# Optimization experiments

Measured on AMD Instinct MI355X. Metric: run time of the kernel, lower is better.

The kernel has to match this reference:

```python
import jax, jax.numpy as jnp
import numpy as np
from jax import lax

C_RED = 32
IN_CH = 256
BN_EPS = 1e-5
NORM_EPS = 1e-6


def setup_inputs() -> dict:
    key = jax.random.key(0)
    ks = jax.random.split(key, 5)
    B, H, W = 16, 64, 64
    x = jax.random.normal(ks[0], (B, IN_CH, H, W), dtype=jnp.float32)
    w_reduce = jax.random.normal(ks[1], (C_RED, IN_CH), dtype=jnp.float32) * 0.05
    bn_gamma = jnp.ones((C_RED,), dtype=jnp.float32)
    bn_beta = jnp.zeros((C_RED,), dtype=jnp.float32)
    bn_mean = jax.random.normal(ks[2], (C_RED,), dtype=jnp.float32) * 0.1
    bn_var = jax.random.uniform(ks[3], (C_RED,), dtype=jnp.float32, minval=0.5, maxval=1.5)
    # depthwise 3x3 kernel, OIHW with I=1 (groups == channels)
    dw_weight = jax.random.normal(ks[4], (C_RED, 1, 3, 3), dtype=jnp.float32) * 0.1
    scale = jnp.ones((C_RED,), dtype=jnp.float32)
    return {"x": x, "w_reduce": w_reduce, "bn_gamma": bn_gamma, "bn_beta": bn_beta,
            "bn_mean": bn_mean, "bn_var": bn_var, "dw_weight": dw_weight, "scale": scale}


def _l2_normalize(t):
    # F.normalize(p=2, dim=1, eps=1e-6): divide by max(||t||_2, eps) along channel dim
    n = jnp.sqrt(jnp.sum(t * t, axis=1, keepdims=True))
    return t / jnp.maximum(n, NORM_EPS)


def reference(x, w_reduce, bn_gamma, bn_beta, bn_mean, bn_var, dw_weight, scale):
    # 1x1 reduce conv (no bias)
    z = jnp.einsum('bihw,oi->bohw', x, w_reduce)
    # BatchNorm2d (inference: running stats)
    inv = bn_gamma / jnp.sqrt(bn_var + BN_EPS)
    z = z * inv[None, :, None, None] + (bn_beta - bn_mean * inv)[None, :, None, None]
    z = jax.nn.relu(z)
    # SpiralTwist: depthwise 3x3 conv (SAME) then per-channel scale
    z_tw = lax.conv_general_dilated(
        z, dw_weight, window_strides=(1, 1), padding='SAME',
        feature_group_count=C_RED,
        dimension_numbers=('NCHW', 'OIHW', 'NCHW'))
    z_tw = z_tw * scale[None, :, None, None]
    z_norm = _l2_normalize(z)
    z_tw_norm = _l2_normalize(z_tw)
    # upper-triangular channel pairs (i <= j)
    idx_i, idx_j = np.triu_indices(C_RED, k=0)
    pair = z_norm[:, idx_i] * z_tw_norm[:, idx_j]  # [B, C*(C+1)/2, H, W]
    return jnp.concatenate([z_norm, pair], axis=1)
```

## Files before the change

### kernel.cpp

```cpp
#include <hip/hip_runtime.h>
#include <stdint.h>

#define CIN  256
#define CR   32
#define COUT 560

__global__ __launch_bounds__(512) void k_conv1x1(
    const float* __restrict__ x,
    const float* __restrict__ wr,
    const float* __restrict__ gamma,
    const float* __restrict__ beta,
    const float* __restrict__ mean,
    const float* __restrict__ var,
    float* __restrict__ z)
{
    const int tid = threadIdx.x;
    const int og  = __builtin_amdgcn_readfirstlane(tid >> 6);
    const int q   = tid & 63;
    const int blk = blockIdx.x;
    const int b   = blk >> 4;
    const int p0  = (blk & 15) << 8;

    const float* xb = x + ((((size_t)b) * CIN) << 12) + p0 + (q << 2);
    const float* wp = wr + og * 4 * CIN;

    float4 a0 = {0.f,0.f,0.f,0.f};
    float4 a1 = {0.f,0.f,0.f,0.f};
    float4 a2 = {0.f,0.f,0.f,0.f};
    float4 a3 = {0.f,0.f,0.f,0.f};

    float4 xv0[16], xv1[16];

#define LOADCH(buf, cc)                                                      \
    _Pragma("unroll")                                                        \
    for (int k = 0; k < 16; ++k)                                             \
        buf[k] = *(const float4*)(xb + ((size_t)((cc) * 16 + k) << 12));

#define FMACH(buf, cc)                                                       \
    _Pragma("unroll")                                                        \
    for (int k = 0; k < 16; ++k) {                                           \
        const int ic = (cc) * 16 + k;                                        \
        const float w0 = wp[           ic];                                  \
        const float w1 = wp[    CIN  + ic];                                  \
        const float w2 = wp[2 * CIN  + ic];                                  \
        const float w3 = wp[3 * CIN  + ic];                                  \
        a0.x = fmaf(buf[k].x, w0, a0.x);  a0.y = fmaf(buf[k].y, w0, a0.y);   \
        a0.z = fmaf(buf[k].z, w0, a0.z);  a0.w = fmaf(buf[k].w, w0, a0.w);   \
        a1.x = fmaf(buf[k].x, w1, a1.x);  a1.y = fmaf(buf[k].y, w1, a1.y);   \
        a1.z = fmaf(buf[k].z, w1, a1.z);  a1.w = fmaf(buf[k].w, w1, a1.w);   \
        a2.x = fmaf(buf[k].x, w2, a2.x);  a2.y = fmaf(buf[k].y, w2, a2.y);   \
        a2.z = fmaf(buf[k].z, w2, a2.z);  a2.w = fmaf(buf[k].w, w2, a2.w);   \
        a3.x = fmaf(buf[k].x, w3, a3.x);  a3.y = fmaf(buf[k].y, w3, a3.y);   \
        a3.z = fmaf(buf[k].z, w3, a3.z);  a3.w = fmaf(buf[k].w, w3, a3.w);   \
    }

    LOADCH(xv0, 0);
    #pragma unroll 1
    for (int cc = 0; cc < 16; cc += 2) {
        LOADCH(xv1, cc + 1);
        FMACH(xv0, cc);
        if (cc + 2 < 16) { LOADCH(xv0, cc + 2); }
        FMACH(xv1, cc + 1);
    }
#undef LOADCH
#undef FMACH

    float4* zq = (float4*)(z + (((size_t)b * CR) << 12) + p0 + (q << 2));
    #pragma unroll
    for (int o = 0; o < 4; ++o) {
        const int oc = og * 4 + o;
        const float inv = gamma[oc] / sqrtf(var[oc] + 1e-5f);
        const float bia = beta[oc] - mean[oc] * inv;
        const float4 a = (o == 0) ? a0 : (o == 1) ? a1 : (o == 2) ? a2 : a3;
        float4 r;
        r.x = fmaxf(fmaf(a.x, inv, bia), 0.f);
        r.y = fmaxf(fmaf(a.y, inv, bia), 0.f);
        r.z = fmaxf(fmaf(a.z, inv, bia), 0.f);
        r.w = fmaxf(fmaf(a.w, inv, bia), 0.f);
        zq[(size_t)oc << 10] = r;
    }
}

__global__ __launch_bounds__(256) void k_twist(
    const float* __restrict__ z,
    const float* __restrict__ dww,
    const float* __restrict__ scl,
    float* __restrict__ out)
{
    __shared__ float4 znl4[CR][64];
    __shared__ float4 ps1[4][64];
    __shared__ float4 ps2[4][64];

    const int tid  = threadIdx.x;
    const int cg   = __builtin_amdgcn_readfirstlane(tid >> 6);
    const int lane = tid & 63;
    const int r    = lane >> 4;
    const int cq   = lane & 15;
    const int blk  = blockIdx.x;
    const int qq   = blk & 3;
    const int sl   = blk >> 2;
    const int b    = sl >> 4;
    const int h0   = (sl & 15) << 2;
    const int hh   = h0 + r;

    const float* zb = z + (((size_t)b * CR) << 12);

    float4 zc[8], tw[8];
    float4 s1 = {0.f,0.f,0.f,0.f};
    float4 s2 = {0.f,0.f,0.f,0.f};

    #pragma unroll
    for (int k = 0; k < 8; ++k) {
        const int c = cg + 4 * k;
        const float* zp = zb + ((size_t)c << 12);
        float4 acc = {0.f,0.f,0.f,0.f};
        float4 ctr = {0.f,0.f,0.f,0.f};
        #pragma unroll
        for (int dy = 0; dy < 3; ++dy) {
            const int hy = hh + dy - 1;
            const bool rok = ((unsigned)hy) < 64u;
            const float* zr = zp + (hy << 6);
            float4 M  = {0.f,0.f,0.f,0.f};
            float4 L4 = {0.f,0.f,0.f,0.f};
            float4 R4 = {0.f,0.f,0.f,0.f};
            if (rok) {
                M = *(const float4*)(zr + (cq << 2));
                if (cq > 0)  L4 = *(const float4*)(zr + (cq << 2) - 4);
                if (cq < 15) R4 = *(const float4*)(zr + (cq << 2) + 4);
            }
            const float w0 = dww[c * 9 + dy * 3 + 0];
            const float w1 = dww[c * 9 + dy * 3 + 1];
            const float w2 = dww[c * 9 + dy * 3 + 2];
            acc.x = fmaf(w0, L4.w, fmaf(w1, M.x, fmaf(w2, M.y, acc.x)));
            acc.y = fmaf(w0, M.x,  fmaf(w1, M.y, fmaf(w2, M.z, acc.y)));
            acc.z = fmaf(w0, M.y,  fmaf(w1, M.z, fmaf(w2, M.w, acc.z)));
            acc.w = fmaf(w0, M.z,  fmaf(w1, M.w, fmaf(w2, R4.x, acc.w)));
            if (dy == 1) ctr = M;
        }
        const float s = scl[c];
        float4 t;
        t.x = acc.x * s;  t.y = acc.y * s;  t.z = acc.z * s;  t.w = acc.w * s;
        zc[k] = ctr;  tw[k] = t;
        s1.x = fmaf(ctr.x, ctr.x, s1.x);  s1.y = fmaf(ctr.y, ctr.y, s1.y);
        s1.z = fmaf(ctr.z, ctr.z, s1.z);  s1.w = fmaf(ctr.w, ctr.w, s1.w);
        s2.x = fmaf(t.x, t.x, s2.x);      s2.y = fmaf(t.y, t.y, s2.y);
        s2.z = fmaf(t.z, t.z, s2.z);      s2.w = fmaf(t.w, t.w, s2.w);
    }

    ps1[cg][lane] = s1;
    ps2[cg][lane] = s2;
    __syncthreads();

    float4 t1, t2;
    {
        const float4 u0 = ps1[0][lane], u1 = ps1[1][lane],
                     u2 = ps1[2][lane], u3 = ps1[3][lane];
        t1.x = u0.x + u1.x + u2.x + u3.x;  t1.y = u0.y + u1.y + u2.y + u3.y;
        t1.z = u0.z + u1.z + u2.z + u3.z;  t1.w = u0.w + u1.w + u2.w + u3.w;
        const float4 v0 = ps2[0][lane], v1 = ps2[1][lane],
                     v2 = ps2[2][lane], v3 = ps2[3][lane];
        t2.x = v0.x + v1.x + v2.x + v3.x;  t2.y = v0.y + v1.y + v2.y + v3.y;
        t2.z = v0.z + v1.z + v2.z + v3.z;  t2.w = v0.w + v1.w + v2.w + v3.w;
    }
    float4 rn1, rn2;
    rn1.x = 1.0f / fmaxf(sqrtf(t1.x), 1e-6f);
    rn1.y = 1.0f / fmaxf(sqrtf(t1.y), 1e-6f);
    rn1.z = 1.0f / fmaxf(sqrtf(t1.z), 1e-6f);
    rn1.w = 1.0f / fmaxf(sqrtf(t1.w), 1e-6f);
    rn2.x = 1.0f / fmaxf(sqrtf(t2.x), 1e-6f);
    rn2.y = 1.0f / fmaxf(sqrtf(t2.y), 1e-6f);
    rn2.z = 1.0f / fmaxf(sqrtf(t2.z), 1e-6f);
    rn2.w = 1.0f / fmaxf(sqrtf(t2.w), 1e-6f);

    float4* outq = (float4*)(out + (((size_t)b * COUT) << 12) + (hh << 6)) + cq;

    #pragma unroll
    for (int k = 0; k < 8; ++k) {
        const int c = cg + 4 * k;
        float4 zn;
        zn.x = zc[k].x * rn1.x;  zn.y = zc[k].y * rn1.y;
        zn.z = zc[k].z * rn1.z;  zn.w = zc[k].w * rn1.w;
        znl4[c][lane] = zn;
        if (qq == 0) outq[(size_t)c << 10] = zn;
        tw[k].x *= rn2.x;  tw[k].y *= rn2.y;
        tw[k].z *= rn2.z;  tw[k].w *= rn2.w;
    }
    __syncthreads();

    #pragma unroll
    for (int k = 0; k < 8; ++k) {
        const int j = cg + 4 * k;
        const float4 t = tw[k];
        const int i0 = (qq * (j + 1)) >> 2;
        const int i1 = ((qq + 1) * (j + 1)) >> 2;
        int P = 32 + j + 31 * i0 - ((i0 * (i0 - 1)) >> 1);
        for (int i = i0; i < i1; ++i) {
            const float4 zi = znl4[i][lane];
            float4 v;
            v.x = zi.x * t.x;  v.y = zi.y * t.y;
            v.z = zi.z * t.z;  v.w = zi.w * t.w;
            outq[(size_t)P << 10] = v;
            P += 31 - i;
        }
    }
}

extern "C" void kernel_launch(void* const* d_in, const int* in_sizes, int n_in,
                              void* d_out, int out_size, void* d_ws, size_t ws_size,
                              hipStream_t stream) {
    const float* x     = (const float*)d_in[0];
    const float* wr    = (const float*)d_in[1];
    const float* gamma = (const float*)d_in[2];
    const float* beta  = (const float*)d_in[3];
    const float* mean  = (const float*)d_in[4];
    const float* var   = (const float*)d_in[5];
    const float* dww   = (const float*)d_in[6];
    const float* scl   = (const float*)d_in[7];
    float* z   = (float*)d_ws;
    float* out = (float*)d_out;

    hipLaunchKernelGGL(k_conv1x1, dim3(256), dim3(512), 0, stream,
                       x, wr, gamma, beta, mean, var, z);
    hipLaunchKernelGGL(k_twist, dim3(1024), dim3(256), 0, stream,
                       z, dww, scl, out);
}
```

Baseline: 234.7 us.

## Remove 4x redundant stencil recompute in twist kernel and use nontemporal stores

The twist kernel previously launched 4 blocks per row slice, each recomputing the full depthwise conv and norms and splitting only the pair-output writes. It now uses one 512-thread block per slice with 8 channel groups, so each block computes the conv once and writes all pair outputs, with an imbalanced per-warp loop over i<=j. All output stores become nontemporal to avoid polluting cache with the large write-once output. The trade-off is 256 blocks instead of 1024, giving less parallelism and uneven warp work.

```diff
diff --git a/kernel.cpp b/kernel.cpp
--- a/kernel.cpp
+++ b/kernel.cpp
@@ -4,6 +4,13 @@
 #define CIN  256
 #define CR   32
 #define COUT 560
+
+typedef float nfloat4 __attribute__((ext_vector_type(4)));
+
+static __device__ __forceinline__ void nt_store4(float4 v, float4* p) {
+    nfloat4 t; t.x = v.x; t.y = v.y; t.z = v.z; t.w = v.w;
+    __builtin_nontemporal_store(t, (nfloat4*)p);
+}
 
 __global__ __launch_bounds__(512) void k_conv1x1(
     const float* __restrict__ x,
@@ -81,15 +88,15 @@
     }
 }
 
-__global__ __launch_bounds__(256) void k_twist(
+__global__ __launch_bounds__(512) void k_twist(
     const float* __restrict__ z,
     const float* __restrict__ dww,
     const float* __restrict__ scl,
     float* __restrict__ out)
 {
     __shared__ float4 znl4[CR][64];
-    __shared__ float4 ps1[4][64];
-    __shared__ float4 ps2[4][64];
+    __shared__ float4 ps1[8][64];
+    __shared__ float4 ps2[8][64];
 
     const int tid  = threadIdx.x;
     const int cg   = __builtin_amdgcn_readfirstlane(tid >> 6);
@@ -97,21 +104,19 @@
     const int r    = lane >> 4;
     const int cq   = lane & 15;
     const int blk  = blockIdx.x;
-    const int qq   = blk & 3;
-    const int sl   = blk >> 2;
-    const int b    = sl >> 4;
-    const int h0   = (sl & 15) << 2;
+    const int b    = blk >> 4;
+    const int h0   = (blk & 15) << 2;
     const int hh   = h0 + r;
 
     const float* zb = z + (((size_t)b * CR) << 12);
 
-    float4 zc[8], tw[8];
+    float4 zc[4], tw[4];
     float4 s1 = {0.f,0.f,0.f,0.f};
     float4 s2 = {0.f,0.f,0.f,0.f};
 
     #pragma unroll
-    for (int k = 0; k < 8; ++k) {
-        const int c = cg + 4 * k;
+    for (int k = 0; k < 4; ++k) {
+        const int c = cg + 8 * k;
         const float* zp = zb + ((size_t)c << 12);
         float4 acc = {0.f,0.f,0.f,0.f};
         float4 ctr = {0.f,0.f,0.f,0.f};
@@ -151,16 +156,14 @@
     ps2[cg][lane] = s2;
     __syncthreads();
 
-    float4 t1, t2;
-    {
-        const float4 u0 = ps1[0][lane], u1 = ps1[1][lane],
-                     u2 = ps1[2][lane], u3 = ps1[3][lane];
-        t1.x = u0.x + u1.x + u2.x + u3.x;  t1.y = u0.y + u1.y + u2.y + u3.y;
-        t1.z = u0.z + u1.z + u2.z + u3.z;  t1.w = u0.w + u1.w + u2.w + u3.w;
-        const float4 v0 = ps2[0][lane], v1 = ps2[1][lane],
-                     v2 = ps2[2][lane], v3 = ps2[3][lane];
-        t2.x = v0.x + v1.x + v2.x + v3.x;  t2.y = v0.y + v1.y + v2.y + v3.y;
-        t2.z = v0.z + v1.z + v2.z + v3.z;  t2.w = v0.w + v1.w + v2.w + v3.w;
+    float4 t1 = {0.f,0.f,0.f,0.f};
+    float4 t2 = {0.f,0.f,0.f,0.f};
+    #pragma unroll
+    for (int g = 0; g < 8; ++g) {
+        const float4 u = ps1[g][lane];
+        t1.x += u.x;  t1.y += u.y;  t1.z += u.z;  t1.w += u.w;
+        const float4 v = ps2[g][lane];
+        t2.x += v.x;  t2.y += v.y;  t2.z += v.z;  t2.w += v.w;
     }
     float4 rn1, rn2;
     rn1.x = 1.0f / fmaxf(sqrtf(t1.x), 1e-6f);
@@ -175,31 +178,29 @@
     float4* outq = (float4*)(out + (((size_t)b * COUT) << 12) + (hh << 6)) + cq;
 
     #pragma unroll
-    for (int k = 0; k < 8; ++k) {
-        const int c = cg + 4 * k;
+    for (int k = 0; k < 4; ++k) {
+        const int c = cg + 8 * k;
         float4 zn;
         zn.x = zc[k].x * rn1.x;  zn.y = zc[k].y * rn1.y;
         zn.z = zc[k].z * rn1.z;  zn.w = zc[k].w * rn1.w;
         znl4[c][lane] = zn;
-        if (qq == 0) outq[(size_t)c << 10] = zn;
+        nt_store4(zn, &outq[(size_t)c << 10]);
         tw[k].x *= rn2.x;  tw[k].y *= rn2.y;
         tw[k].z *= rn2.z;  tw[k].w *= rn2.w;
     }
     __syncthreads();
 
     #pragma unroll
-    for (int k = 0; k < 8; ++k) {
-        const int j = cg + 4 * k;
+    for (int k = 0; k < 4; ++k) {
+        const int j = cg + 8 * k;
         const float4 t = tw[k];
-        const int i0 = (qq * (j + 1)) >> 2;
-        const int i1 = ((qq + 1) * (j + 1)) >> 2;
-        int P = 32 + j + 31 * i0 - ((i0 * (i0 - 1)) >> 1);
-        for (int i = i0; i < i1; ++i) {
+        int P = 32 + j;
+        for (int i = 0; i <= j; ++i) {
             const float4 zi = znl4[i][lane];
             float4 v;
             v.x = zi.x * t.x;  v.y = zi.y * t.y;
             v.z = zi.z * t.z;  v.w = zi.w * t.w;
-            outq[(size_t)P << 10] = v;
+            nt_store4(v, &outq[(size_t)P << 10]);
             P += 31 - i;
         }
     }
@@ -221,6 +222,6 @@
 
     hipLaunchKernelGGL(k_conv1x1, dim3(256), dim3(512), 0, stream,
                        x, wr, gamma, beta, mean, var, z);
-    hipLaunchKernelGGL(k_twist, dim3(1024), dim3(256), 0, stream,
+    hipLaunchKernelGGL(k_twist, dim3(256), dim3(512), 0, stream,
                        z, dww, scl, out);
 }
```

After: 231.2 us. No clear change (-1.5%).
